# Performance work log

Measured on AMD Instinct MI355X. Metric: run time of the kernel, lower is better.

Reference implementation:

```python
import jax, jax.numpy as jnp
import numpy as np

K = 11      # kernel_size
PAD = 5     # (dilation*(K-1)+1 - 1)//2 with dilation=1


def _unfold(x, k, pad):
    # torch nn.Unfold ordering: channel slowest, then (ki, kj) fastest.
    B, C, H, W = x.shape
    xp = jnp.pad(x, ((0, 0), (0, 0), (pad, pad), (pad, pad)))
    # [B, C, k*k, H, W] -- small fixed loop over the 121 kernel offsets
    cols = jnp.stack([xp[:, :, i:i + H, j:j + W]
                      for i in range(k) for j in range(k)], axis=2)
    return cols.reshape(B, C * k * k, H * W)  # [B, 363, L]


def setup_inputs() -> dict:
    key = jax.random.key(0)
    ks = jax.random.split(key, 4)
    x = jax.random.normal(ks[0], (1, 3, 400, 400), dtype=jnp.float32)
    W1 = jax.random.normal(ks[1], (363, 128), dtype=jnp.float32) * 0.05
    b1 = jnp.zeros((128,), dtype=jnp.float32)
    W2 = jax.random.normal(ks[2], (128, 64), dtype=jnp.float32) * 0.08
    b2 = jnp.zeros((64,), dtype=jnp.float32)
    W3 = jax.random.normal(ks[3], (64, 8), dtype=jnp.float32) * 0.1
    b3 = jnp.zeros((8,), dtype=jnp.float32)
    return {"x": x, "W1": W1, "b1": b1, "W2": W2, "b2": b2, "W3": W3, "b3": b3}


def reference(x, W1, b1, W2, b2, W3, b3):
    B, C, H, W = x.shape
    cols = _unfold(x, K, PAD)                 # [B, 363, H*W]
    h = cols.transpose(0, 2, 1)               # [B, L, 363]
    h = jax.nn.leaky_relu(h @ W1 + b1)        # [B, L, 128], slope 0.01 = torch default
    h = jax.nn.leaky_relu(h @ W2 + b2)        # [B, L, 64]
    h = h @ W3 + b3                           # [B, L, 8]
    # Fold(kernel=1) is a reshape; squeeze(0) + permute -> [H, W, E]
    y = h[0].reshape(H, W, -1)
    # F.normalize(p=2, dim=-1, eps=1e-12)
    n = jnp.maximum(jnp.linalg.norm(y, axis=-1, keepdims=True), 1e-12)
    return y / n
```

## Files before the change

### kernel.cpp

```cpp
#include <hip/hip_runtime.h>
#include <hip/hip_bf16.h>
#include <math.h>

typedef _Float16 f16x8 __attribute__((ext_vector_type(8)));
typedef _Float16 f16x4 __attribute__((ext_vector_type(4)));
typedef float    f32x4 __attribute__((ext_vector_type(4)));

#define IMG   400
#define NPIX  160000
#define NKT1  18
#define W1P   (NKT1*8*64*8)
#define W2P   (4*4*64*8)
#define W3P   (2*64*8)
#define HSS   40
#define XPH   1938

__device__ __forceinline__ void async_cp16(const _Float16* g, _Float16* l) {
    __builtin_amdgcn_global_load_lds(
        (const __attribute__((address_space(1))) uint32_t*)g,
        (__attribute__((address_space(3))) uint32_t*)l, 16, 0, 0);
}

__global__ void pack_weights(const float* __restrict__ W1,
                             const float* __restrict__ W2,
                             const float* __restrict__ W3,
                             _Float16* __restrict__ ws)
{
    int i = blockIdx.x * blockDim.x + threadIdx.x;
    if (i < 576 * 128) {
        int kp = i >> 7, n = i & 127;
        int kt = kp >> 5, kl = kp & 31, q = kl >> 3, j = kl & 7;
        int pair = kp >> 4, kj = kp & 15;
        int c = pair / 12, ki = pair % 12;
        int mt = n >> 4, n15 = n & 15;
        int lane = q * 16 + n15;
        float v = (ki < 11 && kj < 11) ? W1[(c * 121 + ki * 11 + kj) * 128 + n] : 0.0f;
        ws[((kt * 8 + mt) * 64 + lane) * 8 + j] = (_Float16)v;
    } else if (i < 576 * 128 + 128 * 64) {
        int e = i - 576 * 128;
        int kp = e >> 6, n = e & 63;
        int kt = kp >> 5, kl = kp & 31, q = kl >> 3, j = kl & 7;
        int mt = n >> 4, n15 = n & 15;
        int lane = q * 16 + n15;
        ws[W1P + ((kt * 4 + mt) * 64 + lane) * 8 + j] = (_Float16)W2[kp * 64 + n];
    } else if (i < 576 * 128 + 128 * 64 + 64 * 16) {
        int e = i - 576 * 128 - 128 * 64;
        int kp = e >> 4, n = e & 15;
        int kt = kp >> 5, kl = kp & 31, q = kl >> 3, j = kl & 7;
        int lane = q * 16 + n;
        float v = (n < 8) ? W3[kp * 8 + n] : 0.0f;
        ws[W1P + W2P + (kt * 64 + lane) * 8 + j] = (_Float16)v;
    }
}

__global__ __launch_bounds__(256, 4) void fused_unfold_mlp(
    const float* __restrict__ x,
    const float* __restrict__ b1,
    const float* __restrict__ b2,
    const float* __restrict__ b3,
    const _Float16* __restrict__ wpack,
    float* __restrict__ out)
{
    __shared__ __align__(16) _Float16 xs[2 * XPH];
    __shared__ __align__(16) _Float16 w1s[2 * 4096];
    __shared__ __align__(16) _Float16 hs[4][32 * HSS];

    const int tid  = threadIdx.x;
    const int wave = tid >> 6;
    const int lane = tid & 63;
    const int q    = lane >> 4;
    const int n15  = lane & 15;
    const int bx   = blockIdx.x;
    const int by   = blockIdx.y;

    const _Float16* w1p = wpack;
    const _Float16* w2p = wpack + W1P;
    const _Float16* w3p = wpack + W1P + W2P;

    const int kt0 = (bx + by * 25) % NKT1;

    {
        int seg = wave * 2;
        async_cp16(w1p + kt0 * 4096 + seg * 512 + lane * 8, &w1s[seg * 512]);
        async_cp16(w1p + kt0 * 4096 + (seg + 1) * 512 + lane * 8, &w1s[(seg + 1) * 512]);
    }

    for (int w = tid; w < 3 * 19 * 35; w += 256) {
        int col = w % 35;
        int rc  = w / 35;
        int row = rc % 19, c = rc / 19;
        int gy = by * 8 + row - 5;
        int gx = bx * 16 + col - 6;
        float v = 0.0f;
        if ((unsigned)gy < (unsigned)IMG && (unsigned)gx < (unsigned)IMG)
            v = x[c * NPIX + gy * IMG + gx];
        _Float16 hv = (_Float16)v;
        int base = (c * 19 + row) * 34;
        if (col >= 1)  xs[base + col - 1] = hv;
        if (col <= 33) xs[XPH + base + col] = hv;
    }
    __syncthreads();

    const uint32_t* xsd = (const uint32_t*)xs;
    const int h = q >> 1;
    const int u = n15 + (n15 & 1) + ((q & 1) << 3);
    const int bdw0 = (n15 & 1) * (XPH / 2) + (u >> 1);
    int bdwt[2];
#pragma unroll
    for (int t = 0; t < 2; ++t)
        bdwt[t] = bdw0 + (wave * 2 + t + h) * 17;

    f32x4 acc1[2][8];
#pragma unroll
    for (int t = 0; t < 2; ++t)
#pragma unroll
        for (int mt = 0; mt < 8; ++mt)
            acc1[t][mt] = (f32x4){0.f, 0.f, 0.f, 0.f};

    int kt = kt0;
    for (int kk = 0; kk < NKT1; ++kk) {
        if (kk) __syncthreads();
        const int buf  = kk & 1;
        const int nbuf = buf ^ 1;
        const int ktn  = (kt + 1 == NKT1) ? 0 : kt + 1;
        if (kk < NKT1 - 1) {
            int seg = wave * 2;
            async_cp16(w1p + ktn * 4096 + seg * 512 + lane * 8,
                       &w1s[nbuf * 4096 + seg * 512]);
            async_cp16(w1p + ktn * 4096 + (seg + 1) * 512 + lane * 8,
                       &w1s[nbuf * 4096 + (seg + 1) * 512]);
        }

        const int d6  = (kt >= 12) ? 2 : (kt >= 6 ? 1 : 0);
        const int m6  = kt - d6 * 6;
        const int rim = (d6 * 19 + 2 * m6) * 17;

        f16x8 bf[2];
#pragma unroll
        for (int t = 0; t < 2; ++t) {
            union { uint32_t u[4]; f16x8 f; } cv;
#pragma unroll
            for (int m = 0; m < 4; ++m)
                cv.u[m] = xsd[bdwt[t] + rim + m];
            bf[t] = cv.f;
        }
        const _Float16* wb = &w1s[buf * 4096];
#pragma unroll
        for (int mt = 0; mt < 8; ++mt) {
            f16x8 af = *(const f16x8*)(wb + (mt * 64 + lane) * 8);
            acc1[0][mt] = __builtin_amdgcn_mfma_f32_16x16x32_f16(af, bf[0], acc1[0][mt], 0, 0, 0);
            acc1[1][mt] = __builtin_amdgcn_mfma_f32_16x16x32_f16(af, bf[1], acc1[1][mt], 0, 0, 0);
        }
        kt = ktn;
    }

    _Float16* hw = hs[wave];

    f32x4 acc2[2][4];
#pragma unroll
    for (int t = 0; t < 2; ++t)
#pragma unroll
        for (int mt = 0; mt < 4; ++mt)
            acc2[t][mt] = (f32x4){0.f, 0.f, 0.f, 0.f};

#pragma unroll
    for (int k2 = 0; k2 < 4; ++k2) {
#pragma unroll
        for (int lm = 0; lm < 2; ++lm) {
            int mt = 2 * k2 + lm;
            float4 bb = *(const float4*)(b1 + mt * 16 + q * 4);
#pragma unroll
            for (int t = 0; t < 2; ++t) {
                f16x4 hv;
#pragma unroll
                for (int r = 0; r < 4; ++r) {
                    float v = acc1[t][mt][r] + ((const float*)&bb)[r];
                    v = fmaxf(v, 0.01f * v);
                    hv[r] = (_Float16)v;
                }
                *(f16x4*)(hw + (t * 16 + n15) * HSS + lm * 16 + q * 4) = hv;
            }
        }
        f16x8 bf[2];
#pragma unroll
        for (int t = 0; t < 2; ++t)
            bf[t] = *(const f16x8*)(hw + (t * 16 + n15) * HSS + q * 8);
#pragma unroll
        for (int mt2 = 0; mt2 < 4; ++mt2) {
            f16x8 af = *(const f16x8*)(w2p + ((k2 * 4 + mt2) * 64 + lane) * 8);
            acc2[0][mt2] = __builtin_amdgcn_mfma_f32_16x16x32_f16(af, bf[0], acc2[0][mt2], 0, 0, 0);
            acc2[1][mt2] = __builtin_amdgcn_mfma_f32_16x16x32_f16(af, bf[1], acc2[1][mt2], 0, 0, 0);
        }
    }

    f16x8 af3[2];
#pragma unroll
    for (int k3 = 0; k3 < 2; ++k3)
        af3[k3] = *(const f16x8*)(w3p + (k3 * 64 + lane) * 8);

    f32x4 acc3[2];
    acc3[0] = (f32x4){0.f, 0.f, 0.f, 0.f};
    acc3[1] = (f32x4){0.f, 0.f, 0.f, 0.f};
#pragma unroll
    for (int k3 = 0; k3 < 2; ++k3) {
#pragma unroll
        for (int lm = 0; lm < 2; ++lm) {
            int mt2 = 2 * k3 + lm;
            float4 bb = *(const float4*)(b2 + mt2 * 16 + q * 4);
#pragma unroll
            for (int t = 0; t < 2; ++t) {
                f16x4 hv;
#pragma unroll
                for (int r = 0; r < 4; ++r) {
                    float v = acc2[t][mt2][r] + ((const float*)&bb)[r];
                    v = fmaxf(v, 0.01f * v);
                    hv[r] = (_Float16)v;
                }
                *(f16x4*)(hw + (t * 16 + n15) * HSS + lm * 16 + q * 4) = hv;
            }
        }
#pragma unroll
        for (int t = 0; t < 2; ++t) {
            f16x8 bf = *(const f16x8*)(hw + (t * 16 + n15) * HSS + q * 8);
            acc3[t] = __builtin_amdgcn_mfma_f32_16x16x32_f16(af3[k3], bf, acc3[t], 0, 0, 0);
        }
    }

    float4 bb3 = make_float4(0.f, 0.f, 0.f, 0.f);
    if (q < 2) bb3 = *(const float4*)(b3 + q * 4);
#pragma unroll
    for (int t = 0; t < 2; ++t) {
        float v0 = acc3[t][0] + bb3.x;
        float v1 = acc3[t][1] + bb3.y;
        float v2 = acc3[t][2] + bb3.z;
        float v3 = acc3[t][3] + bb3.w;
        float s = v0 * v0 + v1 * v1 + v2 * v2 + v3 * v3;
        s += __shfl_xor(s, 16);
        s += __shfl_xor(s, 32);
        float inv = 1.0f / fmaxf(sqrtf(s), 1e-12f);
        if (q < 2) {
            int p = (by * 8 + wave * 2 + t) * IMG + bx * 16 + n15;
            float4 o = make_float4(v0 * inv, v1 * inv, v2 * inv, v3 * inv);
            *(float4*)(out + p * 8 + q * 4) = o;
        }
    }
}

extern "C" void kernel_launch(void* const* d_in, const int* in_sizes, int n_in,
                              void* d_out, int out_size, void* d_ws, size_t ws_size,
                              hipStream_t stream) {
    const float* x  = (const float*)d_in[0];
    const float* W1 = (const float*)d_in[1];
    const float* b1 = (const float*)d_in[2];
    const float* W2 = (const float*)d_in[3];
    const float* b2 = (const float*)d_in[4];
    const float* W3 = (const float*)d_in[5];
    const float* b3 = (const float*)d_in[6];
    float* out = (float*)d_out;
    _Float16* ws = (_Float16*)d_ws;

    pack_weights<<<dim3(324), dim3(256), 0, stream>>>(W1, W2, W3, ws);
    fused_unfold_mlp<<<dim3(25, 50), dim3(256), 0, stream>>>(x, b1, b2, b3, ws, out);
}
```

Baseline: 98.87 us.

## Deepen W1 LDS prefetch to four buffers with explicit vmcnt waits

Replaces the double-buffered W1 staging with a four-slot ring that keeps up to three K-chunks in flight. Each iteration uses a manual s_waitcnt vmcnt(2) plus s_barrier instead of a full __syncthreads, and the last two chunks run after the loop. The aim is to hide global-to-LDS load latency behind the MFMA work. In exchange, W1 LDS use doubles and launch bounds drop from 4 to 3 blocks per CU, which may cut occupancy.

Result: no change. 98.71 us (-0.2%).

```diff
diff --git a/kernel.cpp b/kernel.cpp
--- a/kernel.cpp
+++ b/kernel.cpp
@@ -53,7 +53,7 @@
     }
 }
 
-__global__ __launch_bounds__(256, 4) void fused_unfold_mlp(
+__global__ __launch_bounds__(256, 3) void fused_unfold_mlp(
     const float* __restrict__ x,
     const float* __restrict__ b1,
     const float* __restrict__ b2,
@@ -62,7 +62,7 @@
     float* __restrict__ out)
 {
     __shared__ __align__(16) _Float16 xs[2 * XPH];
-    __shared__ __align__(16) _Float16 w1s[2 * 4096];
+    __shared__ __align__(16) _Float16 w1s[4 * 4096];
     __shared__ __align__(16) _Float16 hs[4][32 * HSS];
 
     const int tid  = threadIdx.x;
@@ -79,11 +79,15 @@
 
     const int kt0 = (bx + by * 25) % NKT1;
 
-    {
+    auto issue_chunk = [&](int ktv, int b) {
         int seg = wave * 2;
-        async_cp16(w1p + kt0 * 4096 + seg * 512 + lane * 8, &w1s[seg * 512]);
-        async_cp16(w1p + kt0 * 4096 + (seg + 1) * 512 + lane * 8, &w1s[(seg + 1) * 512]);
-    }
+        async_cp16(w1p + ktv * 4096 + seg * 512 + lane * 8,
+                   &w1s[b * 4096 + seg * 512]);
+        async_cp16(w1p + ktv * 4096 + (seg + 1) * 512 + lane * 8,
+                   &w1s[b * 4096 + (seg + 1) * 512]);
+    };
+
+    issue_chunk(kt0, 0);
 
     for (int w = tid; w < 3 * 19 * 35; w += 256) {
         int col = w % 35;
@@ -101,6 +105,13 @@
     }
     __syncthreads();
 
+    {
+        int kt1 = (kt0 + 1 >= NKT1) ? kt0 + 1 - NKT1 : kt0 + 1;
+        int kt2 = (kt0 + 2 >= NKT1) ? kt0 + 2 - NKT1 : kt0 + 2;
+        issue_chunk(kt1, 1);
+        issue_chunk(kt2, 2);
+    }
+
     const uint32_t* xsd = (const uint32_t*)xs;
     const int h = q >> 1;
     const int u = n15 + (n15 & 1) + ((q & 1) << 3);
@@ -117,24 +128,10 @@
         for (int mt = 0; mt < 8; ++mt)
             acc1[t][mt] = (f32x4){0.f, 0.f, 0.f, 0.f};
 
-    int kt = kt0;
-    for (int kk = 0; kk < NKT1; ++kk) {
-        if (kk) __syncthreads();
-        const int buf  = kk & 1;
-        const int nbuf = buf ^ 1;
-        const int ktn  = (kt + 1 == NKT1) ? 0 : kt + 1;
-        if (kk < NKT1 - 1) {
-            int seg = wave * 2;
-            async_cp16(w1p + ktn * 4096 + seg * 512 + lane * 8,
-                       &w1s[nbuf * 4096 + seg * 512]);
-            async_cp16(w1p + ktn * 4096 + (seg + 1) * 512 + lane * 8,
-                       &w1s[nbuf * 4096 + (seg + 1) * 512]);
-        }
-
-        const int d6  = (kt >= 12) ? 2 : (kt >= 6 ? 1 : 0);
-        const int m6  = kt - d6 * 6;
+    auto compute_chunk = [&](int ktv, int b) {
+        const int d6  = (ktv >= 12) ? 2 : (ktv >= 6 ? 1 : 0);
+        const int m6  = ktv - d6 * 6;
         const int rim = (d6 * 19 + 2 * m6) * 17;
-
         f16x8 bf[2];
 #pragma unroll
         for (int t = 0; t < 2; ++t) {
@@ -144,15 +141,31 @@
                 cv.u[m] = xsd[bdwt[t] + rim + m];
             bf[t] = cv.f;
         }
-        const _Float16* wb = &w1s[buf * 4096];
+        const _Float16* wb = &w1s[b * 4096];
 #pragma unroll
         for (int mt = 0; mt < 8; ++mt) {
             f16x8 af = *(const f16x8*)(wb + (mt * 64 + lane) * 8);
             acc1[0][mt] = __builtin_amdgcn_mfma_f32_16x16x32_f16(af, bf[0], acc1[0][mt], 0, 0, 0);
             acc1[1][mt] = __builtin_amdgcn_mfma_f32_16x16x32_f16(af, bf[1], acc1[1][mt], 0, 0, 0);
         }
-        kt = ktn;
-    }
+    };
+
+    int kt  = kt0;
+    int kt3 = (kt0 + 3 >= NKT1) ? kt0 + 3 - NKT1 : kt0 + 3;
+    for (int kk = 0; kk < 16; ++kk) {
+        asm volatile("s_waitcnt vmcnt(2)" ::: "memory");
+        asm volatile("s_barrier" ::: "memory");
+        if (kk < 15)
+            issue_chunk(kt3, (kk + 3) & 3);
+        compute_chunk(kt, kk & 3);
+        kt  = (kt  + 1 == NKT1) ? 0 : kt  + 1;
+        kt3 = (kt3 + 1 == NKT1) ? 0 : kt3 + 1;
+    }
+    asm volatile("s_waitcnt vmcnt(0)" ::: "memory");
+    asm volatile("s_barrier" ::: "memory");
+    compute_chunk(kt, 0);
+    kt = (kt + 1 == NKT1) ? 0 : kt + 1;
+    compute_chunk(kt, 1);
 
     _Float16* hw = hs[wave];
 
```
